# Optimization experiments

Measured on AMD Instinct MI355X. Metric: run time of the kernel, lower is better.

## Reference

```python
import jax, jax.numpy as jnp
import numpy as np

# Model dims (DeepSeek-V2-Lite-like)
M = 2048          # tokens (batch*seq flattened)
H = 1024          # hidden_size
E = 64            # n_routed_experts
N = 1024          # moe_intermediate_size
N_GROUP = 8       # n_group
TOPK_GROUP = 3    # topk_group
TOPK = 6          # num_experts_per_tok
N_SHARED = 2      # n_shared_experts
IS = N_SHARED * N # shared-expert intermediate size
ROUTED_SCALING = 1.0
RENORMALIZE = False  # norm_topk_prob


def setup_inputs() -> dict:
    key = jax.random.key(0)
    k = jax.random.split(key, 6)
    s = 0.02
    return {
        "x": jax.random.normal(k[0], (M, H), dtype=jnp.float32),
        "gate_w": jax.random.normal(k[1], (E, H), dtype=jnp.float32) * s,
        "w1": jax.random.normal(k[2], (E, 2 * N, H), dtype=jnp.float32) * s,  # [gate; up]
        "w2": jax.random.normal(k[3], (E, H, N), dtype=jnp.float32) * s,
        "shared_gate_up": jax.random.normal(k[4], (2 * IS, H), dtype=jnp.float32) * s,
        "shared_down": jax.random.normal(k[5], (H, IS), dtype=jnp.float32) * s,
    }


def grouped_topk(scores):
    # scores: [M, E] post-softmax router probabilities
    m = scores.shape[0]
    group_scores = scores.reshape(m, N_GROUP, E // N_GROUP).max(axis=-1)  # [M, G]
    _, group_idx = jax.lax.top_k(group_scores, TOPK_GROUP)                # [M, topk_group]
    rows = jnp.arange(m)[:, None]
    group_mask = jnp.zeros_like(group_scores).at[rows, group_idx].set(1.0)
    score_mask = jnp.broadcast_to(group_mask[:, :, None], (m, N_GROUP, E // N_GROUP)).reshape(m, E)
    tmp = jnp.where(score_mask.astype(bool), scores, 0.0)
    topk_w, topk_ids = jax.lax.top_k(tmp, TOPK)
    if RENORMALIZE:
        topk_w = topk_w / jnp.sum(topk_w, axis=-1, keepdims=True)
    return topk_w, topk_ids


def reference(x, gate_w, w1, w2, shared_gate_up, shared_down):
    m = x.shape[0]
    # Router: softmax scores -> group-masked top-k
    scores = jax.nn.softmax(x @ gate_w.T, axis=-1)          # [M, E]
    topk_w, topk_ids = grouped_topk(scores)                 # [M, K]
    # Combine weights per (token, expert); equivalent to per-slot weighted sum
    rows = jnp.arange(m)[:, None]
    combine = jnp.zeros((m, E), x.dtype).at[rows, topk_ids].add(topk_w)  # [M, E]

    # Fused experts: gate/up GEMM -> silu_and_mul -> down GEMM, weighted sum over experts
    def step(acc, we):
        w1_e, w2_e, c_e = we                    # [2N,H], [H,N], [M]
        gu = x @ w1_e.T                         # [M, 2N]
        h = jax.nn.silu(gu[:, :N]) * gu[:, N:]  # silu_and_mul -> [M, N]
        return acc + c_e[:, None] * (h @ w2_e.T), None

    out, _ = jax.lax.scan(step, jnp.zeros_like(x), (w1, w2, combine.T))
    out = out * ROUTED_SCALING

    # Shared experts MLP (DeepseekV2MLP, silu)
    gu = x @ shared_gate_up.T                   # [M, 2*IS]
    shared = (jax.nn.silu(gu[:, :IS]) * gu[:, IS:]) @ shared_down.T  # [M, H]
    return out + shared
```

## Files before the change

kernel.cpp:

```cpp
#include <hip/hip_runtime.h>
#include <stdint.h>

#define M_TOK 2048
#define HID   1024
#define NEXP  64
#define TOPK  6
#define TOTSLOT (M_TOK*TOPK)

typedef unsigned short u16;
typedef __attribute__((ext_vector_type(4))) u16   u16x4;
typedef __attribute__((ext_vector_type(8))) u16   u16x8;
typedef __attribute__((ext_vector_type(4))) float f32x4;
typedef __attribute__((ext_vector_type(8))) short bf16x8;

__device__ __forceinline__ u16 f2b(float f) {
    union { float f; uint32_t u; } v; v.f = f;
    uint32_t r = v.u + 0x7FFFu + ((v.u >> 16) & 1u);
    return (u16)(r >> 16);
}
__device__ __forceinline__ float b2f(u16 b) {
    union { uint32_t u; float f; } v; v.u = ((uint32_t)b) << 16; return v.f;
}

__global__ __launch_bounds__(256) void prep_kernel(const float* __restrict__ x,
                                                   u16* __restrict__ xb,
                                                   const float* __restrict__ gw,
                                                   float* __restrict__ gwT) {
    int b = blockIdx.x;
    if (b < 2048) {
        int i = (b * 256 + threadIdx.x) * 4;
        float4 v = *reinterpret_cast<const float4*>(x + i);
        u16x4 o; o[0] = f2b(v.x); o[1] = f2b(v.y); o[2] = f2b(v.z); o[3] = f2b(v.w);
        *reinterpret_cast<u16x4*>(xb + i) = o;
    } else {
        int i = (b - 2048) * 256 + threadIdx.x;
        int e = i >> 10, k = i & 1023;
        gwT[k * NEXP + e] = gw[i];
    }
}

__global__ __launch_bounds__(64) void router_kernel(
    const float* __restrict__ x, const float* __restrict__ gwT,
    int* __restrict__ topk_id, float* __restrict__ topk_w, int* __restrict__ counts)
{
    int t = blockIdx.x, lane = threadIdx.x;
    __shared__ float xr[HID];
    for (int k = lane; k < HID; k += 64) xr[k] = x[(size_t)t * HID + k];
    __syncthreads();
    double s0 = 0.0, s1 = 0.0, s2 = 0.0, s3 = 0.0;
    for (int k = 0; k < HID; k += 4) {
        s0 += (double)xr[k]   * (double)gwT[(k)   * NEXP + lane];
        s1 += (double)xr[k+1] * (double)gwT[(k+1) * NEXP + lane];
        s2 += (double)xr[k+2] * (double)gwT[(k+2) * NEXP + lane];
        s3 += (double)xr[k+3] * (double)gwT[(k+3) * NEXP + lane];
    }
    double s = (s0 + s1) + (s2 + s3);
    __shared__ double lg[NEXP];
    __shared__ float  pr[NEXP];
    float sf = (float)s;
    float mx = sf;
    for (int o = 32; o; o >>= 1) mx = fmaxf(mx, __shfl_xor(mx, o));
    float ev = __expf(sf - mx);
    float sum = ev;
    for (int o = 32; o; o >>= 1) sum += __shfl_xor(sum, o);
    lg[lane] = s; pr[lane] = ev / sum;
    __syncthreads();
    if (lane == 0) {
        double gs[8];
        #pragma unroll
        for (int g = 0; g < 8; ++g) {
            double m = lg[g*8];
            #pragma unroll
            for (int i = 1; i < 8; ++i) m = fmax(m, lg[g*8+i]);
            gs[g] = m;
        }
        unsigned gsel = 0;
        for (int r = 0; r < 3; ++r) {
            int bi = 0; double bv = -1e300;
            for (int g = 0; g < 8; ++g)
                if (!((gsel>>g)&1u) && gs[g] > bv) { bv = gs[g]; bi = g; }
            gsel |= 1u << bi;
        }
        unsigned long long taken = 0;
        for (int r = 0; r < TOPK; ++r) {
            int bi = 0; double bv = -1e300;
            for (int e = 0; e < NEXP; ++e) {
                if (!((gsel >> (e>>3)) & 1u)) continue;
                if ((taken >> e) & 1ull) continue;
                if (lg[e] > bv) { bv = lg[e]; bi = e; }
            }
            taken |= 1ull << bi;
            topk_id[t*TOPK + r] = bi;
            topk_w[t*TOPK + r] = pr[bi];
            atomicAdd(&counts[bi], 1);
        }
    }
}

__global__ void scan_kernel(const int* __restrict__ counts, int* __restrict__ offs,
                            int* __restrict__ cursor) {
    if (threadIdx.x == 0) {
        int acc = 0;
        for (int e = 0; e < NEXP; ++e) { offs[e] = acc; cursor[e] = acc; acc += counts[e]; }
        offs[NEXP] = acc;
    }
}

__global__ __launch_bounds__(256) void fill_kernel(
    const int* __restrict__ topk_id, const float* __restrict__ topk_w,
    int* __restrict__ cursor, int* __restrict__ stok, float* __restrict__ sw,
    int* __restrict__ spos)
{
    int idx = blockIdx.x*256 + threadIdx.x;
    if (idx >= TOTSLOT) return;
    int e = topk_id[idx];
    int pos = atomicAdd(&cursor[e], 1);
    stok[pos] = idx / TOPK;
    sw[pos] = topk_w[idx];
    spos[idx] = pos;
}

template<int KIND>
__device__ __forceinline__ void gemm_core(
    const int e, const int my, const int nblk,
    const u16* __restrict__ A, const float* __restrict__ Bw,
    u16* __restrict__ Hout, float* __restrict__ Out,
    const int* __restrict__ offs, const int* __restrict__ stok,
    const float* __restrict__ sw,
    u16* __restrict__ AsR, u16* __restrict__ BsR,
    int* __restrict__ tkl, float* __restrict__ swl)
{
    constexpr bool G1     = (KIND == 0 || KIND == 1);
    constexpr bool ROUTED = (KIND == 0 || KIND == 2);
    constexpr int  BM     = 128;
    constexpr int  KD     = (KIND == 3) ? 2048 : 1024;
    constexpr int  KITER  = KD / 64;
    constexpr int  NPAIR  = (KIND == 0) ? 1024 : 2048;

    const int tid  = threadIdx.x;
    const int lane = tid & 63;
    const int wv   = tid >> 6;

    int off = 0, cnt = M_TOK;
    if (ROUTED) { off = offs[e]; cnt = offs[e+1] - off; }
    const int m0 = my * BM;
    if (m0 >= cnt) return;

    if (ROUTED && tid < BM) {
        int gr = m0 + tid;
        if (KIND == 0) {
            tkl[tid] = (gr < cnt) ? stok[off + gr] : 0;
            swl[tid] = (gr < cnt) ? sw[off + gr] : 0.f;
        } else {
            int r = off + gr; if (r > TOTSLOT-1) r = TOTSLOT-1;
            tkl[tid] = r;
        }
    }
    __syncthreads();

    const int acol8 = (lane & 7) ^ (lane >> 3);
    int aoff[2];
    #pragma unroll
    for (int j = 0; j < 2; ++j) {
        int r = wv*16 + j*8 + (lane >> 3);
        int arow = ROUTED ? tkl[r] : (m0 + r);
        aoff[j] = arow * KD + acol8 * 8;
    }

    const float* Be = Bw;
    if (KIND == 0) Be += (size_t)e * (size_t)(2*1024*1024);
    if (KIND == 2) Be += (size_t)e * (size_t)(1024*1024);
    const int rb = tid >> 2;
    const int q  = tid & 3;
    int brow;
    if (G1) brow = (rb < 64) ? (nblk*64 + rb) : (NPAIR + nblk*64 + (rb - 64));
    else    brow = nblk*128 + rb;
    const float* bsrc = Be + (size_t)brow * KD + q*16;

    float4 br[4];

    auto stageA = [&](int buf, int k0) {
        #pragma unroll
        for (int j = 0; j < 2; ++j) {
            __builtin_amdgcn_global_load_lds(
                (const __attribute__((address_space(1))) uint32_t*)(A + (size_t)(aoff[j] + k0)),
                (__attribute__((address_space(3))) uint32_t*)(AsR + buf*(BM*64) + (wv*16 + j*8)*64),
                16, 0, 0);
        }
    };
    auto loadB = [&](int k0) {
        #pragma unroll
        for (int j = 0; j < 4; ++j)
            br[j] = *reinterpret_cast<const float4*>(bsrc + k0 + j*4);
    };
    auto storeB = [&](int buf) {
        char* bd = (char*)(BsR + buf*(128*64)) + rb*128;
        #pragma unroll
        for (int half = 0; half < 2; ++half) {
            u16x8 w;
            w[0] = f2b(br[2*half].x);   w[1] = f2b(br[2*half].y);
            w[2] = f2b(br[2*half].z);   w[3] = f2b(br[2*half].w);
            w[4] = f2b(br[2*half+1].x); w[5] = f2b(br[2*half+1].y);
            w[6] = f2b(br[2*half+1].z); w[7] = f2b(br[2*half+1].w);
            int ch = q*2 + half;
            *reinterpret_cast<u16x8*>(bd + ((ch ^ (rb & 7)) << 4)) = w;
        }
    };

    f32x4 acc[8];
    #pragma unroll
    for (int nf = 0; nf < 8; ++nf) acc[nf] = (f32x4){0.f, 0.f, 0.f, 0.f};

    auto mfma_phase = [&](int buf) {
        const char* Ab = (const char*)(AsR + buf*(BM*64));
        const char* Bb = (const char*)(BsR + buf*(128*64));
        #pragma unroll
        for (int kk = 0; kk < 2; ++kk) {
            const int sc = kk*4 + (lane >> 4);
            const int ra = wv*16 + (lane & 15);
            bf16x8 af = *reinterpret_cast<const bf16x8*>(Ab + ra*128 + ((sc ^ (ra & 7)) << 4));
            #pragma unroll
            for (int nf = 0; nf < 8; ++nf) {
                int rbb = nf*16 + (lane & 15);
                bf16x8 bfr = *reinterpret_cast<const bf16x8*>(Bb + rbb*128 + ((sc ^ (rbb & 7)) << 4));
                acc[nf] = __builtin_amdgcn_mfma_f32_16x16x32_bf16(af, bfr, acc[nf], 0, 0, 0);
            }
        }
    };

    stageA(0, 0);
    loadB(0);
    storeB(0);
    __syncthreads();

    for (int kt = 0; kt < KITER; ++kt) {
        const int cur = kt & 1, nxt = cur ^ 1;
        const bool more = (kt + 1 < KITER);
        if (more) { stageA(nxt, (kt + 1) * 64); loadB((kt + 1) * 64); }
        mfma_phase(cur);
        if (more) storeB(nxt);
        __syncthreads();
    }

    if constexpr (G1) {
        const int colbase = nblk*64 + (lane & 15);
        #pragma unroll
        for (int j = 0; j < 4; ++j) {
            int r = wv*16 + (lane >> 4)*4 + j;
            if (ROUTED && (m0 + r) >= cnt) continue;
            float wgt = (KIND == 0) ? swl[r] : 1.0f;
            size_t orow = (size_t)(ROUTED ? (off + m0 + r) : (m0 + r));
            #pragma unroll
            for (int nf = 0; nf < 4; ++nf) {
                float g = acc[nf][j];
                float u = acc[nf+4][j];
                float hv = (g / (1.f + __expf(-g))) * u * wgt;
                Hout[orow * NPAIR + colbase + nf*16] = f2b(hv);
            }
        }
    } else {
        const int colbase = nblk*128 + (lane & 15);
        #pragma unroll
        for (int j = 0; j < 4; ++j) {
            int r = wv*16 + (lane >> 4)*4 + j;
            if (ROUTED && (m0 + r) >= cnt) continue;
            #pragma unroll
            for (int nf = 0; nf < 8; ++nf) {
                float v = acc[nf][j];
                if (KIND == 2) Hout[(size_t)(off + m0 + r) * HID + colbase + nf*16] = f2b(v);
                else           Out[(size_t)(m0 + r) * HID + colbase + nf*16] = v;
            }
        }
    }
}

__global__ __launch_bounds__(512, 4) void gemm01_kernel(
    const u16* __restrict__ xb, const float* __restrict__ w1, const float* __restrict__ sgu,
    u16* __restrict__ h, u16* __restrict__ hs,
    const int* __restrict__ offs, const int* __restrict__ stok, const float* __restrict__ sw)
{
    __shared__ u16 AsR[2*128*64];
    __shared__ u16 BsR[2*128*64];
    __shared__ int   tkl[128];
    __shared__ float swl[128];
    const int rid = blockIdx.x;
    if (rid < 2048) {
        int slot = rid >> 3;
        int e = (rid & 7) * 8 + (slot >> 5);
        int sub = slot & 31;
        gemm_core<0>(e, sub & 1, sub >> 1, xb, w1, h, nullptr, offs, stok, sw, AsR, BsR, tkl, swl);
    } else {
        int sid = rid - 2048;
        int slot = sid >> 3;
        gemm_core<1>(0, slot & 15, (sid & 7) * 4 + (slot >> 4), xb, sgu, hs, nullptr,
                     offs, stok, sw, AsR, BsR, tkl, swl);
    }
}

__global__ __launch_bounds__(512, 4) void gemm23_kernel(
    const u16* __restrict__ h, const u16* __restrict__ hs,
    const float* __restrict__ w2, const float* __restrict__ sdn,
    u16* __restrict__ y, float* __restrict__ out,
    const int* __restrict__ offs, const int* __restrict__ stok, const float* __restrict__ sw)
{
    __shared__ u16 AsR[2*128*64];
    __shared__ u16 BsR[2*128*64];
    __shared__ int   tkl[128];
    __shared__ float swl[128];
    const int rid = blockIdx.x;
    if (rid >= 128) {
        int r2 = rid - 128;
        int slot = r2 >> 3;
        int e = (r2 & 7) * 8 + (slot >> 4);
        int sub = slot & 15;
        gemm_core<2>(e, sub & 1, sub >> 1, h, w2, y, nullptr, offs, stok, sw, AsR, BsR, tkl, swl);
    } else {
        int slot = rid >> 3;
        gemm_core<3>(0, slot, rid & 7, hs, sdn, nullptr, out,
                     offs, stok, sw, AsR, BsR, tkl, swl);
    }
}

__global__ __launch_bounds__(256) void reduce_kernel(
    const u16* __restrict__ y, const int* __restrict__ spos, float* __restrict__ out)
{
    int t = blockIdx.x;
    int c = threadIdx.x * 4;
    float4 o = *reinterpret_cast<const float4*>(out + (size_t)t*HID + c);
    #pragma unroll
    for (int k = 0; k < TOPK; ++k) {
        int p = spos[t*TOPK + k];
        u16x4 v = *reinterpret_cast<const u16x4*>(y + (size_t)p*HID + c);
        o.x += b2f(v[0]); o.y += b2f(v[1]); o.z += b2f(v[2]); o.w += b2f(v[3]);
    }
    *reinterpret_cast<float4*>(out + (size_t)t*HID + c) = o;
}

extern "C" void kernel_launch(void* const* d_in, const int* in_sizes, int n_in,
                              void* d_out, int out_size, void* d_ws, size_t ws_size,
                              hipStream_t stream)
{
    const float* x   = (const float*)d_in[0];
    const float* gw  = (const float*)d_in[1];
    const float* w1  = (const float*)d_in[2];
    const float* w2  = (const float*)d_in[3];
    const float* sgu = (const float*)d_in[4];
    const float* sdn = (const float*)d_in[5];
    float* out = (float*)d_out;

    char* p = (char*)d_ws;
    auto carve = [&](size_t bytes) { char* r = p; p += (bytes + 255) & ~(size_t)255; return r; };
    u16*   xb      = (u16*)  carve((size_t)M_TOK * HID * 2);
    u16*   h       = (u16*)  carve((size_t)TOTSLOT * 1024 * 2);
    u16*   hs      = (u16*)  carve((size_t)M_TOK * 2048 * 2);
    u16*   y       = (u16*)  carve((size_t)TOTSLOT * HID * 2);
    float* gwT     = (float*)carve((size_t)HID * NEXP * 4);
    int*   topk_id = (int*)  carve(M_TOK * TOPK * 4);
    float* topk_w  = (float*)carve(M_TOK * TOPK * 4);
    int*   counts  = (int*)  carve(NEXP * 4);
    int*   offs    = (int*)  carve((NEXP + 1) * 4);
    int*   cursor  = (int*)  carve(NEXP * 4);
    int*   stok    = (int*)  carve(TOTSLOT * 4);
    float* sw      = (float*)carve(TOTSLOT * 4);
    int*   spos    = (int*)  carve(TOTSLOT * 4);

    hipMemsetAsync(counts, 0, NEXP * 4, stream);
    prep_kernel<<<2304, 256, 0, stream>>>(x, xb, gw, gwT);
    router_kernel<<<M_TOK, 64, 0, stream>>>(x, gwT, topk_id, topk_w, counts);
    scan_kernel<<<1, 64, 0, stream>>>(counts, offs, cursor);
    fill_kernel<<<(TOTSLOT + 255)/256, 256, 0, stream>>>(topk_id, topk_w, cursor, stok, sw, spos);

    gemm01_kernel<<<2560, 512, 0, stream>>>(xb, w1, sgu, h, hs, offs, stok, sw);
    gemm23_kernel<<<1152, 512, 0, stream>>>(h, hs, w2, sdn, y, out, offs, stok, sw);
    reduce_kernel<<<M_TOK, 256, 0, stream>>>(y, spos, out);
}
```

Before: 473.6 us.

## Load A fragments directly to registers, drop A LDS staging, raise occupancy

```diff
diff --git a/kernel.cpp b/kernel.cpp
--- a/kernel.cpp
+++ b/kernel.cpp
@@ -127,8 +127,7 @@
     u16* __restrict__ Hout, float* __restrict__ Out,
     const int* __restrict__ offs, const int* __restrict__ stok,
     const float* __restrict__ sw,
-    u16* __restrict__ AsR, u16* __restrict__ BsR,
-    int* __restrict__ tkl, float* __restrict__ swl)
+    u16* __restrict__ BsR, int* __restrict__ tkl, float* __restrict__ swl)
 {
     constexpr bool G1     = (KIND == 0 || KIND == 1);
     constexpr bool ROUTED = (KIND == 0 || KIND == 2);
@@ -158,14 +157,9 @@
     }
     __syncthreads();
 
-    const int acol8 = (lane & 7) ^ (lane >> 3);
-    int aoff[2];
-    #pragma unroll
-    for (int j = 0; j < 2; ++j) {
-        int r = wv*16 + j*8 + (lane >> 3);
-        int arow = ROUTED ? tkl[r] : (m0 + r);
-        aoff[j] = arow * KD + acol8 * 8;
-    }
+    const int ra = wv*16 + (lane & 15);
+    const int arow = ROUTED ? tkl[ra] : (m0 + ra);
+    const u16* Aq = A + (size_t)arow * KD + (lane >> 4) * 8;
 
     const float* Be = Bw;
     if (KIND == 0) Be += (size_t)e * (size_t)(2*1024*1024);
@@ -178,16 +172,8 @@
     const float* bsrc = Be + (size_t)brow * KD + q*16;
 
     float4 br[4];
-
-    auto stageA = [&](int buf, int k0) {
-        #pragma unroll
-        for (int j = 0; j < 2; ++j) {
-            __builtin_amdgcn_global_load_lds(
-                (const __attribute__((address_space(1))) uint32_t*)(A + (size_t)(aoff[j] + k0)),
-                (__attribute__((address_space(3))) uint32_t*)(AsR + buf*(BM*64) + (wv*16 + j*8)*64),
-                16, 0, 0);
-        }
-    };
+    bf16x8 afE[2], afO[2];
+
     auto loadB = [&](int k0) {
         #pragma unroll
         for (int j = 0; j < 4; ++j)
@@ -206,39 +192,42 @@
             *reinterpret_cast<u16x8*>(bd + ((ch ^ (rb & 7)) << 4)) = w;
         }
     };
+    auto loadA = [&](bf16x8 (&af)[2], int k0) {
+        af[0] = *reinterpret_cast<const bf16x8*>(Aq + k0);
+        af[1] = *reinterpret_cast<const bf16x8*>(Aq + k0 + 32);
+    };
 
     f32x4 acc[8];
     #pragma unroll
     for (int nf = 0; nf < 8; ++nf) acc[nf] = (f32x4){0.f, 0.f, 0.f, 0.f};
 
-    auto mfma_phase = [&](int buf) {
-        const char* Ab = (const char*)(AsR + buf*(BM*64));
+    auto mfma_phase = [&](bf16x8 (&af)[2], int buf) {
         const char* Bb = (const char*)(BsR + buf*(128*64));
         #pragma unroll
         for (int kk = 0; kk < 2; ++kk) {
             const int sc = kk*4 + (lane >> 4);
-            const int ra = wv*16 + (lane & 15);
-            bf16x8 af = *reinterpret_cast<const bf16x8*>(Ab + ra*128 + ((sc ^ (ra & 7)) << 4));
             #pragma unroll
             for (int nf = 0; nf < 8; ++nf) {
                 int rbb = nf*16 + (lane & 15);
                 bf16x8 bfr = *reinterpret_cast<const bf16x8*>(Bb + rbb*128 + ((sc ^ (rbb & 7)) << 4));
-                acc[nf] = __builtin_amdgcn_mfma_f32_16x16x32_bf16(af, bfr, acc[nf], 0, 0, 0);
+                acc[nf] = __builtin_amdgcn_mfma_f32_16x16x32_bf16(af[kk], bfr, acc[nf], 0, 0, 0);
             }
         }
     };
 
-    stageA(0, 0);
     loadB(0);
+    loadA(afE, 0);
     storeB(0);
     __syncthreads();
 
-    for (int kt = 0; kt < KITER; ++kt) {
-        const int cur = kt & 1, nxt = cur ^ 1;
-        const bool more = (kt + 1 < KITER);
-        if (more) { stageA(nxt, (kt + 1) * 64); loadB((kt + 1) * 64); }
-        mfma_phase(cur);
-        if (more) storeB(nxt);
+    for (int kt = 0; kt < KITER; kt += 2) {
+        if (kt + 1 < KITER) { loadB((kt + 1) * 64); loadA(afO, (kt + 1) * 64); }
+        mfma_phase(afE, 0);
+        if (kt + 1 < KITER) storeB(1);
+        __syncthreads();
+        if (kt + 2 < KITER) { loadB((kt + 2) * 64); loadA(afE, (kt + 2) * 64); }
+        mfma_phase(afO, 1);
+        if (kt + 2 < KITER) storeB(0);
         __syncthreads();
     }
 
@@ -274,12 +263,11 @@
     }
 }
 
-__global__ __launch_bounds__(512, 4) void gemm01_kernel(
+__global__ __launch_bounds__(512, 6) void gemm01_kernel(
     const u16* __restrict__ xb, const float* __restrict__ w1, const float* __restrict__ sgu,
     u16* __restrict__ h, u16* __restrict__ hs,
     const int* __restrict__ offs, const int* __restrict__ stok, const float* __restrict__ sw)
 {
-    __shared__ u16 AsR[2*128*64];
     __shared__ u16 BsR[2*128*64];
     __shared__ int   tkl[128];
     __shared__ float swl[128];
@@ -288,22 +276,21 @@
         int slot = rid >> 3;
         int e = (rid & 7) * 8 + (slot >> 5);
         int sub = slot & 31;
-        gemm_core<0>(e, sub & 1, sub >> 1, xb, w1, h, nullptr, offs, stok, sw, AsR, BsR, tkl, swl);
+        gemm_core<0>(e, sub >> 4, sub & 15, xb, w1, h, nullptr, offs, stok, sw, BsR, tkl, swl);
     } else {
         int sid = rid - 2048;
         int slot = sid >> 3;
         gemm_core<1>(0, slot & 15, (sid & 7) * 4 + (slot >> 4), xb, sgu, hs, nullptr,
-                     offs, stok, sw, AsR, BsR, tkl, swl);
-    }
-}
-
-__global__ __launch_bounds__(512, 4) void gemm23_kernel(
+                     offs, stok, sw, BsR, tkl, swl);
+    }
+}
+
+__global__ __launch_bounds__(512, 6) void gemm23_kernel(
     const u16* __restrict__ h, const u16* __restrict__ hs,
     const float* __restrict__ w2, const float* __restrict__ sdn,
     u16* __restrict__ y, float* __restrict__ out,
     const int* __restrict__ offs, const int* __restrict__ stok, const float* __restrict__ sw)
 {
-    __shared__ u16 AsR[2*128*64];
     __shared__ u16 BsR[2*128*64];
     __shared__ int   tkl[128];
     __shared__ float swl[128];
@@ -313,11 +300,11 @@
         int slot = r2 >> 3;
         int e = (r2 & 7) * 8 + (slot >> 4);
         int sub = slot & 15;
-        gemm_core<2>(e, sub & 1, sub >> 1, h, w2, y, nullptr, offs, stok, sw, AsR, BsR, tkl, swl);
+        gemm_core<2>(e, sub >> 3, sub & 7, h, w2, y, nullptr, offs, stok, sw, BsR, tkl, swl);
     } else {
         int slot = rid >> 3;
         gemm_core<3>(0, slot, rid & 7, hs, sdn, nullptr, out,
-                     offs, stok, sw, AsR, BsR, tkl, swl);
+                     offs, stok, sw, BsR, tkl, swl);
     }
 }
 
```

Result: slower. 509.7 us (+7.6%).
